# Performance work log

Measured on AMD Instinct MI355X. Metric: run time of the kernel, lower is better.

The kernel has to match this reference:

```python
import jax, jax.numpy as jnp
import numpy as np
from jax import lax

EPS = 1e-5


def _bn(x, gamma, beta, mean, var):
    # x: [B,C,H,W]; params: [C]
    inv = gamma / jnp.sqrt(var + EPS)
    return x * inv[None, :, None, None] + (beta - mean * inv)[None, :, None, None]


def _conv1x1(x, w):
    # w: [O, C] pointwise conv
    return jnp.einsum('oc,bchw->bohw', w, x)


def setup_inputs() -> dict:
    dim, num_heads = 256, 8
    B, H, W = 4, 40, 40
    key = jax.random.key(0)
    ks = jax.random.split(key, 12)
    inp = {
        'x': jax.random.normal(ks[0], (B, dim, H, W), jnp.float32),
        # qkv: Conv(dim, 2*dim, k=1) = conv1x1 (no bias) + BN + SiLU
        'qkv_w': jax.random.normal(ks[1], (2 * dim, dim), jnp.float32) * 0.05,
        'qkv_gamma': jax.random.uniform(ks[2], (2 * dim,), jnp.float32, 0.5, 1.5),
        'qkv_beta': jax.random.normal(ks[3], (2 * dim,), jnp.float32) * 0.05,
        'qkv_mean': jax.random.normal(ks[4], (2 * dim,), jnp.float32) * 0.05,
        'qkv_var': jax.random.uniform(ks[5], (2 * dim,), jnp.float32, 0.5, 1.5),
        # proj: Conv(dim, dim, k=1)
        'proj_w': jax.random.normal(ks[6], (dim, dim), jnp.float32) * 0.05,
        'proj_gamma': jax.random.uniform(ks[7], (dim,), jnp.float32, 0.5, 1.5),
        'proj_beta': jax.random.normal(ks[8], (dim,), jnp.float32) * 0.05,
        'proj_mean': jax.random.normal(ks[9], (dim,), jnp.float32) * 0.05,
        'proj_var': jax.random.uniform(ks[10], (dim,), jnp.float32, 0.5, 1.5),
        # pe: depthwise 3x3 conv (groups=dim, no bias) + BN (no activation)
        'pe_w': jax.random.normal(ks[11], (dim, 1, 3, 3), jnp.float32) * 0.1,
        'pe_gamma': jax.random.uniform(jax.random.fold_in(key, 100), (dim,), jnp.float32, 0.5, 1.5),
        'pe_beta': jax.random.normal(jax.random.fold_in(key, 101), (dim,), jnp.float32) * 0.05,
        'pe_mean': jax.random.normal(jax.random.fold_in(key, 102), (dim,), jnp.float32) * 0.05,
        'pe_var': jax.random.uniform(jax.random.fold_in(key, 103), (dim,), jnp.float32, 0.5, 1.5),
    }
    return inp


def reference(x, qkv_w, qkv_gamma, qkv_beta, qkv_mean, qkv_var,
              proj_w, proj_gamma, proj_beta, proj_mean, proj_var,
              pe_w, pe_gamma, pe_beta, pe_mean, pe_var):
    B, C, H, W = x.shape
    num_heads = 8
    head_dim = C // num_heads
    N = H * W

    # positional encoding: depthwise 3x3 conv + BN
    pe = lax.conv_general_dilated(
        x, pe_w, window_strides=(1, 1), padding='SAME',
        feature_group_count=C, dimension_numbers=('NCHW', 'OIHW', 'NCHW'))
    pe = _bn(pe, pe_gamma, pe_beta, pe_mean, pe_var)

    # qkv: 1x1 conv + BN + SiLU, then split into q, k along channels
    qkv = jax.nn.silu(_bn(_conv1x1(x, qkv_w), qkv_gamma, qkv_beta, qkv_mean, qkv_var))
    q, k = qkv[:, :C], qkv[:, C:]
    v = x + pe

    # reshape to heads: q,v -> [B,h,N,d]; k -> [B,h,d,N]
    q = q.reshape(B, num_heads, head_dim, N).transpose(0, 1, 3, 2)
    k = k.reshape(B, num_heads, head_dim, N)
    v = v.reshape(B, num_heads, head_dim, N).transpose(0, 1, 3, 2)

    scale = head_dim ** (-0.5)
    attn = jnp.einsum('bhnd,bhdm->bhnm', q, k) * scale  # [B,h,N,N]
    attn = jax.nn.softmax(attn, axis=-1)
    out = jnp.einsum('bhnm,bhmd->bhnd', attn, v)        # [B,h,N,d]
    out = out.transpose(0, 1, 3, 2).reshape(B, C, H, W)

    # proj: 1x1 conv + BN + SiLU
    return jax.nn.silu(_bn(_conv1x1(out, proj_w), proj_gamma, proj_beta, proj_mean, proj_var))
```

## Files before the change

kernel.cpp:

```cpp
#include <hip/hip_runtime.h>
#include <hip/hip_bf16.h>

typedef __attribute__((ext_vector_type(8))) short short8;
typedef __attribute__((ext_vector_type(4))) float f32x4;

__device__ __forceinline__ unsigned short f2bf(float f){
    union { float f; unsigned u; } uf; uf.f = f;
    unsigned u = uf.u;
    u += 0x7FFFu + ((u >> 16) & 1u);
    return (unsigned short)(u >> 16);
}
__device__ __forceinline__ int pack2(float a, float b){
    union { float f; unsigned u; } ua, ub; ua.f = a; ub.f = b;
    unsigned x = ua.u; x += 0x7FFFu + ((x >> 16) & 1u);
    unsigned y = ub.u; y += 0x7FFFu + ((y >> 16) & 1u);
    return (int)((x >> 16) | (y & 0xFFFF0000u));
}
__device__ __forceinline__ unsigned cvtpk(float lo, float hi){
    unsigned r;
    asm("v_cvt_pk_bf16_f32 %0, %1, %2" : "=v"(r) : "v"(lo), "v"(hi));
    return r;
}
__device__ __forceinline__ float fexp2(float x){
    return __builtin_amdgcn_exp2f(x);
}

#define N_SPATIAL 1600
#define QSCALE_LOG2E 0.25506601f
#define LSTR 40

__global__ __launch_bounds__(256) void k_head(const float* __restrict__ x,
                                              const float* __restrict__ pw,
                                              const float* __restrict__ pg,
                                              const float* __restrict__ pb,
                                              const float* __restrict__ pm,
                                              const float* __restrict__ pv,
                                              unsigned short* __restrict__ x_t,
                                              unsigned short* __restrict__ v_mf){
    __shared__ float xs[32][163];
    int bi = blockIdx.x;
    int t = threadIdx.x;
    if (bi < 200){
        int b = bi / 50, nc = bi % 50;
        int n0 = nc * 32;
        int c = t;
        unsigned short vals[32];
        const float* src = x + ((size_t)(b*256 + c))*N_SPATIAL + n0;
        #pragma unroll
        for (int j=0;j<8;j++){
            float4 f = *reinterpret_cast<const float4*>(src + j*4);
            vals[j*4+0] = f2bf(f.x); vals[j*4+1] = f2bf(f.y);
            vals[j*4+2] = f2bf(f.z); vals[j*4+3] = f2bf(f.w);
        }
        unsigned short* dst = x_t + ((size_t)b*N_SPATIAL + n0)*256 + c;
        #pragma unroll
        for (int j=0;j<32;j++) dst[(size_t)j*256] = vals[j];
        return;
    }
    int pbi = bi - 200;
    int b = pbi/200, h=(pbi/25)%8, kt=pbi%25;
    int winStart = kt*64 - 48;
    const float* xbase = x + ((size_t)(b*256 + h*32))*N_SPATIAL;
    #pragma unroll
    for (int i=0;i<20;i++){
        int idx = t + i*256;
        int row = idx / 160, col = idx - row*160;
        int n = winStart + col;
        float val = ((unsigned)n < 1600u) ? xbase[(size_t)row*N_SPATIAL + n] : 0.f;
        xs[row][col] = val;
    }
    __syncthreads();

    int f = t>>6, lane = t&63, ql = lane&15, lg = lane>>4;
    int d = (f>>1)*16 + ql;
    int c = h*32 + d;
    float inv = pg[c]*rsqrtf(pv[c]+1e-5f);
    float bias = pb[c]-pm[c]*inv;
    const float* w9 = pw + c*9;
    float w00=w9[0],w01=w9[1],w02=w9[2],w10=w9[3],w11=w9[4],w12=w9[5],w20=w9[6],w21=w9[7],w22=w9[8];
    const float* xr = xs[d];
    union { unsigned short u[8]; int4 i4; } vals;
    #pragma unroll
    for (int j=0;j<8;j++){
        int key = (f&1)*32 + (j>>2)*16 + 4*lg + (j&3);
        int n = kt*64 + key;
        int hh = n/40, ww = n - hh*40;
        int col = key + 48;
        float acc = 0.f;
        if (hh > 0){
            if (ww > 0)  acc += xr[col-41]*w00;
                         acc += xr[col-40]*w01;
            if (ww < 39) acc += xr[col-39]*w02;
        }
        if (ww > 0)  acc += xr[col-1]*w10;
                     acc += xr[col]*w11;
        if (ww < 39) acc += xr[col+1]*w12;
        if (hh < 39){
            if (ww > 0)  acc += xr[col+39]*w20;
                         acc += xr[col+40]*w21;
            if (ww < 39) acc += xr[col+41]*w22;
        }
        float out = xr[col] + acc*inv + bias;
        vals.u[j] = f2bf(out);
    }
    *reinterpret_cast<int4*>(v_mf + ((size_t)(pbi*4 + f)*64 + lane)*8) = vals.i4;
}

__global__ __launch_bounds__(256) void k_qkv2(const unsigned short* __restrict__ x_t,
                                              const float* __restrict__ wq,
                                              const float* __restrict__ g,
                                              const float* __restrict__ be,
                                              const float* __restrict__ mu,
                                              const float* __restrict__ va,
                                              unsigned short* __restrict__ qk_t){
    __shared__ alignas(16) unsigned short a_lds[64*LSTR];
    __shared__ alignas(16) unsigned short b_lds[64*LSTR];
    int bi = blockIdx.x;
    int b = bi / 200, ot = (bi/25) % 8, nt = bi % 25;
    int o0 = ot*64, n0 = nt*64;
    int tid = threadIdx.x, w = tid>>6, lane = tid&63;
    int row = tid>>2, col8 = (tid&3)*8;
    int ql = lane&15, lg = lane>>4;
    f32x4 acc[4];
    #pragma unroll
    for (int t=0;t<4;t++) acc[t] = (f32x4){0.f,0.f,0.f,0.f};
    const float* asrc = wq + (size_t)(o0+row)*256 + col8;
    const unsigned short* bsrc = x_t + ((size_t)b*N_SPATIAL + n0 + row)*256 + col8;
    for (int k0=0; k0<256; k0+=32){
        float4 f0 = *reinterpret_cast<const float4*>(asrc + k0);
        float4 f1 = *reinterpret_cast<const float4*>(asrc + k0 + 4);
        int4 av; av.x = pack2(f0.x,f0.y); av.y = pack2(f0.z,f0.w);
                 av.z = pack2(f1.x,f1.y); av.w = pack2(f1.z,f1.w);
        *reinterpret_cast<int4*>(&a_lds[row*LSTR + col8]) = av;
        *reinterpret_cast<int4*>(&b_lds[row*LSTR + col8]) = *reinterpret_cast<const int4*>(bsrc + k0);
        __syncthreads();
        short8 af = *reinterpret_cast<const short8*>(&a_lds[(16*w + ql)*LSTR + lg*8]);
        #pragma unroll
        for (int t=0;t<4;t++){
            short8 bf = *reinterpret_cast<const short8*>(&b_lds[(16*t + ql)*LSTR + lg*8]);
            acc[t] = __builtin_amdgcn_mfma_f32_16x16x32_bf16(af, bf, acc[t], 0, 0, 0);
        }
        __syncthreads();
    }
    int ob = o0 + 16*w + 4*lg;
    int grp = ob >> 5, d0 = ob & 31;
    float invr[4], b2r[4];
    #pragma unroll
    for (int r=0;r<4;r++){
        int o = ob + r;
        invr[r] = g[o] * rsqrtf(va[o] + 1e-5f);
        b2r[r]  = be[o] - mu[o]*invr[r];
    }
    float qs = (ob < 256) ? QSCALE_LOG2E : 1.0f;
    unsigned short* dstb = qk_t + ((size_t)(b*16 + grp)*N_SPATIAL)*32 + d0;
    #pragma unroll
    for (int t=0;t<4;t++){
        int n = n0 + 16*t + ql;
        float y[4];
        #pragma unroll
        for (int r=0;r<4;r++){
            float z = acc[t][r]*invr[r] + b2r[r];
            y[r] = (z / (1.f + __expf(-z))) * qs;
        }
        uint2 wv = make_uint2((unsigned)pack2(y[0],y[1]), (unsigned)pack2(y[2],y[3]));
        *reinterpret_cast<uint2*>(dstb + (size_t)n*32) = wv;
    }
}

__global__ __launch_bounds__(512) void k_attn7(const unsigned short* __restrict__ qk_t,
                                               const unsigned short* __restrict__ v_mf,
                                               unsigned short* __restrict__ ao_t){
    __shared__ alignas(16) unsigned short k_lds[3][64*40];
    __shared__ alignas(16) unsigned short v_lds[3][2048];
    int l = blockIdx.x;
    int xc = l & 7, j = l >> 3;
    int gg = xc + 8*(j/25);
    int bi = 25*gg + (j%25);
    int b = gg >> 3, h = gg & 7, qt = bi % 25;
    int tid = threadIdx.x, w = tid>>6, lane = tid&63;

    const unsigned short* ksrc = qk_t + ((size_t)(b*16+8+h)*N_SPATIAL)*32;
    const unsigned short* vms  = v_mf + (size_t)(b*200 + h*25)*2048;

    if (w < 4){
        int ql = lane&15, lg = lane>>4;
        int nq = qt*64 + w*16 + ql;
        const unsigned short* qsrc = qk_t + ((size_t)(b*16+h)*N_SPATIAL)*32;
        short8 qf = *reinterpret_cast<const short8*>(qsrc + (size_t)nq*32 + lg*8);
        f32x4 o0 = (f32x4){0.f,0.f,0.f,0.f};
        f32x4 o1 = (f32x4){0.f,0.f,0.f,0.f};
        float Sp = 0.f;

        asm volatile("" ::: "memory");
        __builtin_amdgcn_s_barrier();
        asm volatile("" ::: "memory");

        int cur = 0;
        for (int kt = 0; kt < 25; ++kt){
            const unsigned short* kb = &k_lds[cur][0];
            const unsigned short* vb = &v_lds[cur][0];
            short8 ka0 = *reinterpret_cast<const short8*>(kb + (size_t)( 0 + ql)*40 + lg*8);
            short8 ka1 = *reinterpret_cast<const short8*>(kb + (size_t)(16 + ql)*40 + lg*8);
            short8 ka2 = *reinterpret_cast<const short8*>(kb + (size_t)(32 + ql)*40 + lg*8);
            short8 ka3 = *reinterpret_cast<const short8*>(kb + (size_t)(48 + ql)*40 + lg*8);

            f32x4 z = (f32x4){0.f,0.f,0.f,0.f};
            f32x4 p0 = __builtin_amdgcn_mfma_f32_16x16x32_bf16(ka0, qf, z, 0,0,0);
            f32x4 p1 = __builtin_amdgcn_mfma_f32_16x16x32_bf16(ka1, qf, z, 0,0,0);
            f32x4 p2 = __builtin_amdgcn_mfma_f32_16x16x32_bf16(ka2, qf, z, 0,0,0);
            f32x4 p3 = __builtin_amdgcn_mfma_f32_16x16x32_bf16(ka3, qf, z, 0,0,0);

            #pragma unroll
            for (int r=0;r<4;r++){
                p0[r] = fexp2(p0[r]);
                p1[r] = fexp2(p1[r]);
                p2[r] = fexp2(p2[r]);
                p3[r] = fexp2(p3[r]);
            }
            Sp += ((p0[0]+p0[1])+(p0[2]+p0[3])) + ((p1[0]+p1[1])+(p1[2]+p1[3]))
                + ((p2[0]+p2[1])+(p2[2]+p2[3])) + ((p3[0]+p3[1])+(p3[2]+p3[3]));

            union { int4 i; short8 s8; } pb0, pb1;
            pb0.i = make_int4((int)cvtpk(p0[0],p0[1]), (int)cvtpk(p0[2],p0[3]),
                              (int)cvtpk(p1[0],p1[1]), (int)cvtpk(p1[2],p1[3]));
            pb1.i = make_int4((int)cvtpk(p2[0],p2[1]), (int)cvtpk(p2[2],p2[3]),
                              (int)cvtpk(p3[0],p3[1]), (int)cvtpk(p3[2],p3[3]));

            short8 va0 = *reinterpret_cast<const short8*>(vb +    0 + lane*8);
            short8 va1 = *reinterpret_cast<const short8*>(vb +  512 + lane*8);
            short8 va2 = *reinterpret_cast<const short8*>(vb + 1024 + lane*8);
            short8 va3 = *reinterpret_cast<const short8*>(vb + 1536 + lane*8);

            o0 = __builtin_amdgcn_mfma_f32_16x16x32_bf16(va0, pb0.s8, o0, 0,0,0);
            o0 = __builtin_amdgcn_mfma_f32_16x16x32_bf16(va1, pb1.s8, o0, 0,0,0);
            o1 = __builtin_amdgcn_mfma_f32_16x16x32_bf16(va2, pb0.s8, o1, 0,0,0);
            o1 = __builtin_amdgcn_mfma_f32_16x16x32_bf16(va3, pb1.s8, o1, 0,0,0);

            asm volatile("" ::: "memory");
            __builtin_amdgcn_s_barrier();
            asm volatile("" ::: "memory");
            cur = (cur==2) ? 0 : cur+1;
        }

        Sp += __shfl_xor(Sp, 16);
        Sp += __shfl_xor(Sp, 32);
        float inv = 1.f / Sp;
        size_t rowoff = ((size_t)b*N_SPATIAL + nq)*256 + h*32;
        uint2 w0 = make_uint2((unsigned)pack2(o0[0]*inv, o0[1]*inv),
                              (unsigned)pack2(o0[2]*inv, o0[3]*inv));
        *reinterpret_cast<uint2*>(ao_t + rowoff + 4*lg) = w0;
        uint2 w1 = make_uint2((unsigned)pack2(o1[0]*inv, o1[1]*inv),
                              (unsigned)pack2(o1[2]*inv, o1[3]*inv));
        *reinterpret_cast<uint2*>(ao_t + rowoff + 16 + 4*lg) = w1;
    } else {
        int pi = tid & 255;
        const unsigned short* kg = ksrc + pi*8;
        const unsigned short* vg = vms  + pi*8;
        unsigned short* kd = &k_lds[0][0] + (pi>>2)*40 + (pi&3)*8;
        unsigned short* vd = &v_lds[0][0] + pi*8;

        int4 a0 = *reinterpret_cast<const int4*>(kg);
        int4 b0 = *reinterpret_cast<const int4*>(vg);
        *reinterpret_cast<int4*>(kd) = a0;
        *reinterpret_cast<int4*>(vd) = b0;
        int4 a1 = *reinterpret_cast<const int4*>(kg + 2048);
        int4 b1 = *reinterpret_cast<const int4*>(vg + 2048);
        *reinterpret_cast<int4*>(kd + 2560) = a1;
        *reinterpret_cast<int4*>(vd + 2048) = b1;
        int4 hk = *reinterpret_cast<const int4*>(kg + 4096);
        int4 hv = *reinterpret_cast<const int4*>(vg + 4096);
        asm volatile("s_waitcnt lgkmcnt(0)" ::: "memory");
        __builtin_amdgcn_s_barrier();
        asm volatile("" ::: "memory");

        int wb = 2;
        for (int kt = 0; kt < 25; ++kt){
            if (kt < 23){
                *reinterpret_cast<int4*>(kd + wb*2560) = hk;
                *reinterpret_cast<int4*>(vd + wb*2048) = hv;
            }
            if (kt < 22){
                hk = *reinterpret_cast<const int4*>(kg + (size_t)(kt+3)*2048);
                hv = *reinterpret_cast<const int4*>(vg + (size_t)(kt+3)*2048);
            }
            asm volatile("s_waitcnt lgkmcnt(0)" ::: "memory");
            __builtin_amdgcn_s_barrier();
            asm volatile("" ::: "memory");
            wb = (wb==2) ? 0 : wb+1;
        }
    }
}

__global__ __launch_bounds__(256) void k_proj2(const unsigned short* __restrict__ ao_t,
                                               const float* __restrict__ wp,
                                               const float* __restrict__ g,
                                               const float* __restrict__ be,
                                               const float* __restrict__ mu,
                                               const float* __restrict__ va,
                                               float* __restrict__ out){
    __shared__ alignas(16) unsigned short a_lds[64*LSTR];
    __shared__ alignas(16) unsigned short b_lds[64*LSTR];
    int bi = blockIdx.x;
    int b = bi / 100, ot = (bi/25) % 4, nt = bi % 25;
    int o0 = ot*64, n0 = nt*64;
    int tid = threadIdx.x, w = tid>>6, lane = tid&63;
    int row = tid>>2, col8 = (tid&3)*8;
    int ql = lane&15, lg = lane>>4;
    f32x4 acc[4];
    #pragma unroll
    for (int t=0;t<4;t++) acc[t] = (f32x4){0.f,0.f,0.f,0.f};
    const float* asrc = wp + (size_t)(o0+row)*256 + col8;
    const unsigned short* bsrc = ao_t + ((size_t)b*N_SPATIAL + n0 + row)*256 + col8;
    for (int k0=0; k0<256; k0+=32){
        float4 f0 = *reinterpret_cast<const float4*>(asrc + k0);
        float4 f1 = *reinterpret_cast<const float4*>(asrc + k0 + 4);
        int4 av; av.x = pack2(f0.x,f0.y); av.y = pack2(f0.z,f0.w);
                 av.z = pack2(f1.x,f1.y); av.w = pack2(f1.z,f1.w);
        *reinterpret_cast<int4*>(&a_lds[row*LSTR + col8]) = av;
        *reinterpret_cast<int4*>(&b_lds[row*LSTR + col8]) = *reinterpret_cast<const int4*>(bsrc + k0);
        __syncthreads();
        short8 af = *reinterpret_cast<const short8*>(&a_lds[(16*w + ql)*LSTR + lg*8]);
        #pragma unroll
        for (int t=0;t<4;t++){
            short8 bf = *reinterpret_cast<const short8*>(&b_lds[(16*t + ql)*LSTR + lg*8]);
            acc[t] = __builtin_amdgcn_mfma_f32_16x16x32_bf16(af, bf, acc[t], 0, 0, 0);
        }
        __syncthreads();
    }
    #pragma unroll
    for (int r=0;r<4;r++){
        int o = o0 + 16*w + lg*4 + r;
        float inv = g[o] * rsqrtf(va[o] + 1e-5f);
        float b2  = be[o] - mu[o]*inv;
        float* dst = out + ((size_t)(b*256 + o))*N_SPATIAL;
        #pragma unroll
        for (int t=0;t<4;t++){
            int n = n0 + 16*t + ql;
            float z = acc[t][r]*inv + b2;
            float y = z / (1.f + __expf(-z));
            dst[n] = y;
        }
    }
}

extern "C" void kernel_launch(void* const* d_in, const int* in_sizes, int n_in,
                              void* d_out, int out_size, void* d_ws, size_t ws_size,
                              hipStream_t stream) {
    const float* x      = (const float*)d_in[0];
    const float* qkv_w  = (const float*)d_in[1];
    const float* qkv_g  = (const float*)d_in[2];
    const float* qkv_b  = (const float*)d_in[3];
    const float* qkv_m  = (const float*)d_in[4];
    const float* qkv_v  = (const float*)d_in[5];
    const float* proj_w = (const float*)d_in[6];
    const float* proj_g = (const float*)d_in[7];
    const float* proj_b = (const float*)d_in[8];
    const float* proj_m = (const float*)d_in[9];
    const float* proj_v = (const float*)d_in[10];
    const float* pe_w   = (const float*)d_in[11];
    const float* pe_g   = (const float*)d_in[12];
    const float* pe_b   = (const float*)d_in[13];
    const float* pe_m   = (const float*)d_in[14];
    const float* pe_v   = (const float*)d_in[15];

    char* ws = (char*)d_ws;
    unsigned short* x_t  = (unsigned short*)(ws);
    unsigned short* v_mf = (unsigned short*)(ws + 3276800);
    unsigned short* qk_t = (unsigned short*)(ws + 6553600);
    unsigned short* ao_t = (unsigned short*)(ws + 13107200);
    float* outp = (float*)d_out;

    k_head <<<1000,256, 0, stream>>>(x, pe_w, pe_g, pe_b, pe_m, pe_v, x_t, v_mf);
    k_qkv2 <<<800, 256, 0, stream>>>(x_t, qkv_w, qkv_g, qkv_b, qkv_m, qkv_v, qk_t);
    k_attn7<<<800, 512, 0, stream>>>(qk_t, v_mf, ao_t);
    k_proj2<<<400, 256, 0, stream>>>(ao_t, proj_w, proj_g, proj_b, proj_m, proj_v, outp);
}
```

Before: 59.22 us.

## Stage GEMM K in two 128-wide halves with register prefetch in qkv/proj

```diff
diff --git a/kernel.cpp b/kernel.cpp
--- a/kernel.cpp
+++ b/kernel.cpp
@@ -27,7 +27,7 @@
 
 #define N_SPATIAL 1600
 #define QSCALE_LOG2E 0.25506601f
-#define LSTR 40
+#define GSTR 136
 
 __global__ __launch_bounds__(256) void k_head(const float* __restrict__ x,
                                               const float* __restrict__ pw,
@@ -106,42 +106,93 @@
     *reinterpret_cast<int4*>(v_mf + ((size_t)(pbi*4 + f)*64 + lane)*8) = vals.i4;
 }
 
-__global__ __launch_bounds__(256) void k_qkv2(const unsigned short* __restrict__ x_t,
+__global__ __launch_bounds__(256) void k_qkv3(const unsigned short* __restrict__ x_t,
                                               const float* __restrict__ wq,
                                               const float* __restrict__ g,
                                               const float* __restrict__ be,
                                               const float* __restrict__ mu,
                                               const float* __restrict__ va,
                                               unsigned short* __restrict__ qk_t){
-    __shared__ alignas(16) unsigned short a_lds[64*LSTR];
-    __shared__ alignas(16) unsigned short b_lds[64*LSTR];
+    __shared__ alignas(16) unsigned short a_lds[64*GSTR];
+    __shared__ alignas(16) unsigned short b_lds[64*GSTR];
     int bi = blockIdx.x;
     int b = bi / 200, ot = (bi/25) % 8, nt = bi % 25;
     int o0 = ot*64, n0 = nt*64;
     int tid = threadIdx.x, w = tid>>6, lane = tid&63;
-    int row = tid>>2, col8 = (tid&3)*8;
     int ql = lane&15, lg = lane>>4;
+    int arow = (tid>>5)*2;
+    int aseg = lane&31;
+    int brow4 = (tid>>4);
+    int bseg = lane&15;
+
+    const float* wbase = wq + (size_t)o0*256;
+    const unsigned short* xbase = x_t + ((size_t)b*N_SPATIAL + n0)*256;
+
     f32x4 acc[4];
     #pragma unroll
     for (int t=0;t<4;t++) acc[t] = (f32x4){0.f,0.f,0.f,0.f};
-    const float* asrc = wq + (size_t)(o0+row)*256 + col8;
-    const unsigned short* bsrc = x_t + ((size_t)b*N_SPATIAL + n0 + row)*256 + col8;
-    for (int k0=0; k0<256; k0+=32){
-        float4 f0 = *reinterpret_cast<const float4*>(asrc + k0);
-        float4 f1 = *reinterpret_cast<const float4*>(asrc + k0 + 4);
-        int4 av; av.x = pack2(f0.x,f0.y); av.y = pack2(f0.z,f0.w);
-                 av.z = pack2(f1.x,f1.y); av.w = pack2(f1.z,f1.w);
-        *reinterpret_cast<int4*>(&a_lds[row*LSTR + col8]) = av;
-        *reinterpret_cast<int4*>(&b_lds[row*LSTR + col8]) = *reinterpret_cast<const int4*>(bsrc + k0);
-        __syncthreads();
-        short8 af = *reinterpret_cast<const short8*>(&a_lds[(16*w + ql)*LSTR + lg*8]);
+
+    #pragma unroll
+    for (int i=0;i<8;i++){
+        int row = (tid>>5) + i*8;
+        float4 fv = *reinterpret_cast<const float4*>(wbase + (size_t)row*256 + aseg*4);
+        *reinterpret_cast<uint2*>(&a_lds[row*GSTR + aseg*4]) =
+            make_uint2((unsigned)pack2(fv.x,fv.y), (unsigned)pack2(fv.z,fv.w));
+    }
+    #pragma unroll
+    for (int i=0;i<4;i++){
+        int row = brow4 + i*16;
+        *reinterpret_cast<int4*>(&b_lds[row*GSTR + bseg*8]) =
+            *reinterpret_cast<const int4*>(xbase + (size_t)row*256 + bseg*8);
+    }
+    __syncthreads();
+
+    float4 pa[8]; int4 pbv[4];
+    #pragma unroll
+    for (int i=0;i<8;i++){
+        int row = (tid>>5) + i*8;
+        pa[i] = *reinterpret_cast<const float4*>(wbase + (size_t)row*256 + 128 + aseg*4);
+    }
+    #pragma unroll
+    for (int i=0;i<4;i++){
+        int row = brow4 + i*16;
+        pbv[i] = *reinterpret_cast<const int4*>(xbase + (size_t)row*256 + 128 + bseg*8);
+    }
+
+    #pragma unroll
+    for (int k0=0; k0<128; k0+=32){
+        short8 af = *reinterpret_cast<const short8*>(&a_lds[(16*w + ql)*GSTR + k0 + lg*8]);
         #pragma unroll
         for (int t=0;t<4;t++){
-            short8 bf = *reinterpret_cast<const short8*>(&b_lds[(16*t + ql)*LSTR + lg*8]);
+            short8 bf = *reinterpret_cast<const short8*>(&b_lds[(16*t + ql)*GSTR + k0 + lg*8]);
             acc[t] = __builtin_amdgcn_mfma_f32_16x16x32_bf16(af, bf, acc[t], 0, 0, 0);
         }
-        __syncthreads();
-    }
+    }
+    __syncthreads();
+
+    #pragma unroll
+    for (int i=0;i<8;i++){
+        int row = (tid>>5) + i*8;
+        *reinterpret_cast<uint2*>(&a_lds[row*GSTR + aseg*4]) =
+            make_uint2((unsigned)pack2(pa[i].x,pa[i].y), (unsigned)pack2(pa[i].z,pa[i].w));
+    }
+    #pragma unroll
+    for (int i=0;i<4;i++){
+        int row = brow4 + i*16;
+        *reinterpret_cast<int4*>(&b_lds[row*GSTR + bseg*8]) = pbv[i];
+    }
+    __syncthreads();
+
+    #pragma unroll
+    for (int k0=0; k0<128; k0+=32){
+        short8 af = *reinterpret_cast<const short8*>(&a_lds[(16*w + ql)*GSTR + k0 + lg*8]);
+        #pragma unroll
+        for (int t=0;t<4;t++){
+            short8 bf = *reinterpret_cast<const short8*>(&b_lds[(16*t + ql)*GSTR + k0 + lg*8]);
+            acc[t] = __builtin_amdgcn_mfma_f32_16x16x32_bf16(af, bf, acc[t], 0, 0, 0);
+        }
+    }
+
     int ob = o0 + 16*w + 4*lg;
     int grp = ob >> 5, d0 = ob & 31;
     float invr[4], b2r[4];
@@ -291,42 +342,92 @@
     }
 }
 
-__global__ __launch_bounds__(256) void k_proj2(const unsigned short* __restrict__ ao_t,
+__global__ __launch_bounds__(256) void k_proj3(const unsigned short* __restrict__ ao_t,
                                                const float* __restrict__ wp,
                                                const float* __restrict__ g,
                                                const float* __restrict__ be,
                                                const float* __restrict__ mu,
                                                const float* __restrict__ va,
                                                float* __restrict__ out){
-    __shared__ alignas(16) unsigned short a_lds[64*LSTR];
-    __shared__ alignas(16) unsigned short b_lds[64*LSTR];
+    __shared__ alignas(16) unsigned short a_lds[64*GSTR];
+    __shared__ alignas(16) unsigned short b_lds[64*GSTR];
     int bi = blockIdx.x;
     int b = bi / 100, ot = (bi/25) % 4, nt = bi % 25;
     int o0 = ot*64, n0 = nt*64;
     int tid = threadIdx.x, w = tid>>6, lane = tid&63;
-    int row = tid>>2, col8 = (tid&3)*8;
     int ql = lane&15, lg = lane>>4;
+    int aseg = lane&31;
+    int brow4 = (tid>>4);
+    int bseg = lane&15;
+
+    const float* wbase = wp + (size_t)o0*256;
+    const unsigned short* xbase = ao_t + ((size_t)b*N_SPATIAL + n0)*256;
+
     f32x4 acc[4];
     #pragma unroll
     for (int t=0;t<4;t++) acc[t] = (f32x4){0.f,0.f,0.f,0.f};
-    const float* asrc = wp + (size_t)(o0+row)*256 + col8;
-    const unsigned short* bsrc = ao_t + ((size_t)b*N_SPATIAL + n0 + row)*256 + col8;
-    for (int k0=0; k0<256; k0+=32){
-        float4 f0 = *reinterpret_cast<const float4*>(asrc + k0);
-        float4 f1 = *reinterpret_cast<const float4*>(asrc + k0 + 4);
-        int4 av; av.x = pack2(f0.x,f0.y); av.y = pack2(f0.z,f0.w);
-                 av.z = pack2(f1.x,f1.y); av.w = pack2(f1.z,f1.w);
-        *reinterpret_cast<int4*>(&a_lds[row*LSTR + col8]) = av;
-        *reinterpret_cast<int4*>(&b_lds[row*LSTR + col8]) = *reinterpret_cast<const int4*>(bsrc + k0);
-        __syncthreads();
-        short8 af = *reinterpret_cast<const short8*>(&a_lds[(16*w + ql)*LSTR + lg*8]);
+
+    #pragma unroll
+    for (int i=0;i<8;i++){
+        int row = (tid>>5) + i*8;
+        float4 fv = *reinterpret_cast<const float4*>(wbase + (size_t)row*256 + aseg*4);
+        *reinterpret_cast<uint2*>(&a_lds[row*GSTR + aseg*4]) =
+            make_uint2((unsigned)pack2(fv.x,fv.y), (unsigned)pack2(fv.z,fv.w));
+    }
+    #pragma unroll
+    for (int i=0;i<4;i++){
+        int row = brow4 + i*16;
+        *reinterpret_cast<int4*>(&b_lds[row*GSTR + bseg*8]) =
+            *reinterpret_cast<const int4*>(xbase + (size_t)row*256 + bseg*8);
+    }
+    __syncthreads();
+
+    float4 pa[8]; int4 pbv[4];
+    #pragma unroll
+    for (int i=0;i<8;i++){
+        int row = (tid>>5) + i*8;
+        pa[i] = *reinterpret_cast<const float4*>(wbase + (size_t)row*256 + 128 + aseg*4);
+    }
+    #pragma unroll
+    for (int i=0;i<4;i++){
+        int row = brow4 + i*16;
+        pbv[i] = *reinterpret_cast<const int4*>(xbase + (size_t)row*256 + 128 + bseg*8);
+    }
+
+    #pragma unroll
+    for (int k0=0; k0<128; k0+=32){
+        short8 af = *reinterpret_cast<const short8*>(&a_lds[(16*w + ql)*GSTR + k0 + lg*8]);
         #pragma unroll
         for (int t=0;t<4;t++){
-            short8 bf = *reinterpret_cast<const short8*>(&b_lds[(16*t + ql)*LSTR + lg*8]);
+            short8 bf = *reinterpret_cast<const short8*>(&b_lds[(16*t + ql)*GSTR + k0 + lg*8]);
             acc[t] = __builtin_amdgcn_mfma_f32_16x16x32_bf16(af, bf, acc[t], 0, 0, 0);
         }
-        __syncthreads();
-    }
+    }
+    __syncthreads();
+
+    #pragma unroll
+    for (int i=0;i<8;i++){
+        int row = (tid>>5) + i*8;
+        *reinterpret_cast<uint2*>(&a_lds[row*GSTR + aseg*4]) =
+            make_uint2((unsigned)pack2(pa[i].x,pa[i].y), (unsigned)pack2(pa[i].z,pa[i].w));
+    }
+    #pragma unroll
+    for (int i=0;i<4;i++){
+        int row = brow4 + i*16;
+        *reinterpret_cast<int4*>(&b_lds[row*GSTR + bseg*8]) = pbv[i];
+    }
+    __syncthreads();
+
+    #pragma unroll
+    for (int k0=0; k0<128; k0+=32){
+        short8 af = *reinterpret_cast<const short8*>(&a_lds[(16*w + ql)*GSTR + k0 + lg*8]);
+        #pragma unroll
+        for (int t=0;t<4;t++){
+            short8 bf = *reinterpret_cast<const short8*>(&b_lds[(16*t + ql)*GSTR + k0 + lg*8]);
+            acc[t] = __builtin_amdgcn_mfma_f32_16x16x32_bf16(af, bf, acc[t], 0, 0, 0);
+        }
+    }
+
     #pragma unroll
     for (int r=0;r<4;r++){
         int o = o0 + 16*w + lg*4 + r;
@@ -371,7 +472,7 @@
     float* outp = (float*)d_out;
 
     k_head <<<1000,256, 0, stream>>>(x, pe_w, pe_g, pe_b, pe_m, pe_v, x_t, v_mf);
-    k_qkv2 <<<800, 256, 0, stream>>>(x_t, qkv_w, qkv_g, qkv_b, qkv_m, qkv_v, qk_t);
+    k_qkv3 <<<800, 256, 0, stream>>>(x_t, qkv_w, qkv_g, qkv_b, qkv_m, qkv_v, qk_t);
     k_attn7<<<800, 512, 0, stream>>>(qk_t, v_mf, ao_t);
-    k_proj2<<<400, 256, 0, stream>>>(ao_t, proj_w, proj_g, proj_b, proj_m, proj_v, outp);
-}
+    k_proj3<<<400, 256, 0, stream>>>(ao_t, proj_w, proj_g, proj_b, proj_m, proj_v, outp);
+}
```

Measured after the change: 62.85 us. 1.06x slower.

## Store K in MFMA fragment layout and stream K/V via direct global-to-LDS loads

Applied to the files above, without the earlier changes.

```diff
diff --git a/kernel.cpp b/kernel.cpp
--- a/kernel.cpp
+++ b/kernel.cpp
@@ -23,6 +23,12 @@
 }
 __device__ __forceinline__ float fexp2(float x){
     return __builtin_amdgcn_exp2f(x);
+}
+__device__ __forceinline__ void load_lds16(const void* g, void* l){
+    __builtin_amdgcn_global_load_lds(
+        (const __attribute__((address_space(1))) unsigned int*)g,
+        (__attribute__((address_space(3))) unsigned int*)l,
+        16, 0, 0);
 }
 
 #define N_SPATIAL 1600
@@ -112,7 +118,8 @@
                                               const float* __restrict__ be,
                                               const float* __restrict__ mu,
                                               const float* __restrict__ va,
-                                              unsigned short* __restrict__ qk_t){
+                                              unsigned short* __restrict__ q_t,
+                                              unsigned short* __restrict__ k_mf){
     __shared__ alignas(16) unsigned short a_lds[64*LSTR];
     __shared__ alignas(16) unsigned short b_lds[64*LSTR];
     int bi = blockIdx.x;
@@ -143,7 +150,7 @@
         __syncthreads();
     }
     int ob = o0 + 16*w + 4*lg;
-    int grp = ob >> 5, d0 = ob & 31;
+    int d0 = ob & 31;
     float invr[4], b2r[4];
     #pragma unroll
     for (int r=0;r<4;r++){
@@ -151,144 +158,135 @@
         invr[r] = g[o] * rsqrtf(va[o] + 1e-5f);
         b2r[r]  = be[o] - mu[o]*invr[r];
     }
-    float qs = (ob < 256) ? QSCALE_LOG2E : 1.0f;
-    unsigned short* dstb = qk_t + ((size_t)(b*16 + grp)*N_SPATIAL)*32 + d0;
-    #pragma unroll
-    for (int t=0;t<4;t++){
-        int n = n0 + 16*t + ql;
-        float y[4];
-        #pragma unroll
-        for (int r=0;r<4;r++){
-            float z = acc[t][r]*invr[r] + b2r[r];
-            y[r] = (z / (1.f + __expf(-z))) * qs;
-        }
-        uint2 wv = make_uint2((unsigned)pack2(y[0],y[1]), (unsigned)pack2(y[2],y[3]));
-        *reinterpret_cast<uint2*>(dstb + (size_t)n*32) = wv;
-    }
-}
-
-__global__ __launch_bounds__(512) void k_attn7(const unsigned short* __restrict__ qk_t,
+    if (ob < 256){
+        int grp = ob >> 5;
+        unsigned short* dstb = q_t + ((size_t)(b*8 + grp)*N_SPATIAL)*32 + d0;
+        #pragma unroll
+        for (int t=0;t<4;t++){
+            int n = n0 + 16*t + ql;
+            float y[4];
+            #pragma unroll
+            for (int r=0;r<4;r++){
+                float z = acc[t][r]*invr[r] + b2r[r];
+                y[r] = (z / (1.f + __expf(-z))) * QSCALE_LOG2E;
+            }
+            *reinterpret_cast<uint2*>(dstb + (size_t)n*32) =
+                make_uint2((unsigned)pack2(y[0],y[1]), (unsigned)pack2(y[2],y[3]));
+        }
+    } else {
+        int hh = (ob>>5) - 8;
+        size_t kbase = (size_t)((b*8+hh)*25)*2048;
+        #pragma unroll
+        for (int t=0;t<4;t++){
+            int n = n0 + 16*t + ql;
+            int kt = n>>6, tf = (n>>4)&3, qr = n&15;
+            float y[4];
+            #pragma unroll
+            for (int r=0;r<4;r++){
+                float z = acc[t][r]*invr[r] + b2r[r];
+                y[r] = z / (1.f + __expf(-z));
+            }
+            size_t off = kbase + (size_t)kt*2048 + tf*512 + ((d0>>3)*16 + qr)*8 + (d0&7);
+            *reinterpret_cast<uint2*>(k_mf + off) =
+                make_uint2((unsigned)pack2(y[0],y[1]), (unsigned)pack2(y[2],y[3]));
+        }
+    }
+}
+
+__global__ __launch_bounds__(256) void k_attn8(const unsigned short* __restrict__ q_t,
+                                               const unsigned short* __restrict__ k_mf,
                                                const unsigned short* __restrict__ v_mf,
                                                unsigned short* __restrict__ ao_t){
-    __shared__ alignas(16) unsigned short k_lds[3][64*40];
-    __shared__ alignas(16) unsigned short v_lds[3][2048];
+    __shared__ alignas(16) unsigned short k_lds[4][2048];
+    __shared__ alignas(16) unsigned short v_lds[4][2048];
     int l = blockIdx.x;
     int xc = l & 7, j = l >> 3;
     int gg = xc + 8*(j/25);
-    int bi = 25*gg + (j%25);
-    int b = gg >> 3, h = gg & 7, qt = bi % 25;
+    int b = gg >> 3, h = gg & 7, qt = j % 25;
     int tid = threadIdx.x, w = tid>>6, lane = tid&63;
-
-    const unsigned short* ksrc = qk_t + ((size_t)(b*16+8+h)*N_SPATIAL)*32;
+    int ql = lane&15, lg = lane>>4;
+    int nq = qt*64 + w*16 + ql;
+
+    const unsigned short* qsrc = q_t + ((size_t)(b*8+h)*N_SPATIAL)*32;
+    const unsigned short* kms  = k_mf + (size_t)((b*8+h)*25)*2048;
     const unsigned short* vms  = v_mf + (size_t)(b*200 + h*25)*2048;
 
-    if (w < 4){
-        int ql = lane&15, lg = lane>>4;
-        int nq = qt*64 + w*16 + ql;
-        const unsigned short* qsrc = qk_t + ((size_t)(b*16+h)*N_SPATIAL)*32;
-        short8 qf = *reinterpret_cast<const short8*>(qsrc + (size_t)nq*32 + lg*8);
-        f32x4 o0 = (f32x4){0.f,0.f,0.f,0.f};
-        f32x4 o1 = (f32x4){0.f,0.f,0.f,0.f};
-        float Sp = 0.f;
-
-        asm volatile("" ::: "memory");
+    short8 qf = *reinterpret_cast<const short8*>(qsrc + (size_t)nq*32 + lg*8);
+
+    const unsigned short* kg = kms + w*512 + lane*8;
+    const unsigned short* vg = vms + w*512 + lane*8;
+
+    load_lds16(kg,        &k_lds[0][w*512]);
+    load_lds16(vg,        &v_lds[0][w*512]);
+    load_lds16(kg + 2048, &k_lds[1][w*512]);
+    load_lds16(vg + 2048, &v_lds[1][w*512]);
+
+    f32x4 o0 = (f32x4){0.f,0.f,0.f,0.f};
+    f32x4 o1 = (f32x4){0.f,0.f,0.f,0.f};
+    float Sp = 0.f;
+
+    for (int kt = 0; kt < 25; ++kt){
+        if (kt+2 < 25){
+            int bidx = (kt+2)&3;
+            load_lds16(kg + (size_t)(kt+2)*2048, &k_lds[bidx][w*512]);
+            load_lds16(vg + (size_t)(kt+2)*2048, &v_lds[bidx][w*512]);
+        }
+        if (kt < 23)       asm volatile("s_waitcnt vmcnt(4)" ::: "memory");
+        else if (kt == 23) asm volatile("s_waitcnt vmcnt(2)" ::: "memory");
+        else               asm volatile("s_waitcnt vmcnt(0)" ::: "memory");
         __builtin_amdgcn_s_barrier();
         asm volatile("" ::: "memory");
 
-        int cur = 0;
-        for (int kt = 0; kt < 25; ++kt){
-            const unsigned short* kb = &k_lds[cur][0];
-            const unsigned short* vb = &v_lds[cur][0];
-            short8 ka0 = *reinterpret_cast<const short8*>(kb + (size_t)( 0 + ql)*40 + lg*8);
-            short8 ka1 = *reinterpret_cast<const short8*>(kb + (size_t)(16 + ql)*40 + lg*8);
-            short8 ka2 = *reinterpret_cast<const short8*>(kb + (size_t)(32 + ql)*40 + lg*8);
-            short8 ka3 = *reinterpret_cast<const short8*>(kb + (size_t)(48 + ql)*40 + lg*8);
-
-            f32x4 z = (f32x4){0.f,0.f,0.f,0.f};
-            f32x4 p0 = __builtin_amdgcn_mfma_f32_16x16x32_bf16(ka0, qf, z, 0,0,0);
-            f32x4 p1 = __builtin_amdgcn_mfma_f32_16x16x32_bf16(ka1, qf, z, 0,0,0);
-            f32x4 p2 = __builtin_amdgcn_mfma_f32_16x16x32_bf16(ka2, qf, z, 0,0,0);
-            f32x4 p3 = __builtin_amdgcn_mfma_f32_16x16x32_bf16(ka3, qf, z, 0,0,0);
-
-            #pragma unroll
-            for (int r=0;r<4;r++){
-                p0[r] = fexp2(p0[r]);
-                p1[r] = fexp2(p1[r]);
-                p2[r] = fexp2(p2[r]);
-                p3[r] = fexp2(p3[r]);
-            }
-            Sp += ((p0[0]+p0[1])+(p0[2]+p0[3])) + ((p1[0]+p1[1])+(p1[2]+p1[3]))
-                + ((p2[0]+p2[1])+(p2[2]+p2[3])) + ((p3[0]+p3[1])+(p3[2]+p3[3]));
-
-            union { int4 i; short8 s8; } pb0, pb1;
-            pb0.i = make_int4((int)cvtpk(p0[0],p0[1]), (int)cvtpk(p0[2],p0[3]),
-                              (int)cvtpk(p1[0],p1[1]), (int)cvtpk(p1[2],p1[3]));
-            pb1.i = make_int4((int)cvtpk(p2[0],p2[1]), (int)cvtpk(p2[2],p2[3]),
-                              (int)cvtpk(p3[0],p3[1]), (int)cvtpk(p3[2],p3[3]));
-
-            short8 va0 = *reinterpret_cast<const short8*>(vb +    0 + lane*8);
-            short8 va1 = *reinterpret_cast<const short8*>(vb +  512 + lane*8);
-            short8 va2 = *reinterpret_cast<const short8*>(vb + 1024 + lane*8);
-            short8 va3 = *reinterpret_cast<const short8*>(vb + 1536 + lane*8);
-
-            o0 = __builtin_amdgcn_mfma_f32_16x16x32_bf16(va0, pb0.s8, o0, 0,0,0);
-            o0 = __builtin_amdgcn_mfma_f32_16x16x32_bf16(va1, pb1.s8, o0, 0,0,0);
-            o1 = __builtin_amdgcn_mfma_f32_16x16x32_bf16(va2, pb0.s8, o1, 0,0,0);
-            o1 = __builtin_amdgcn_mfma_f32_16x16x32_bf16(va3, pb1.s8, o1, 0,0,0);
-
-            asm volatile("" ::: "memory");
-            __builtin_amdgcn_s_barrier();
-            asm volatile("" ::: "memory");
-            cur = (cur==2) ? 0 : cur+1;
-        }
-
-        Sp += __shfl_xor(Sp, 16);
-        Sp += __shfl_xor(Sp, 32);
-        float inv = 1.f / Sp;
-        size_t rowoff = ((size_t)b*N_SPATIAL + nq)*256 + h*32;
-        uint2 w0 = make_uint2((unsigned)pack2(o0[0]*inv, o0[1]*inv),
-                              (unsigned)pack2(o0[2]*inv, o0[3]*inv));
-        *reinterpret_cast<uint2*>(ao_t + rowoff + 4*lg) = w0;
-        uint2 w1 = make_uint2((unsigned)pack2(o1[0]*inv, o1[1]*inv),
-                              (unsigned)pack2(o1[2]*inv, o1[3]*inv));
-        *reinterpret_cast<uint2*>(ao_t + rowoff + 16 + 4*lg) = w1;
-    } else {
-        int pi = tid & 255;
-        const unsigned short* kg = ksrc + pi*8;
-        const unsigned short* vg = vms  + pi*8;
-        unsigned short* kd = &k_lds[0][0] + (pi>>2)*40 + (pi&3)*8;
-        unsigned short* vd = &v_lds[0][0] + pi*8;
-
-        int4 a0 = *reinterpret_cast<const int4*>(kg);
-        int4 b0 = *reinterpret_cast<const int4*>(vg);
-        *reinterpret_cast<int4*>(kd) = a0;
-        *reinterpret_cast<int4*>(vd) = b0;
-        int4 a1 = *reinterpret_cast<const int4*>(kg + 2048);
-        int4 b1 = *reinterpret_cast<const int4*>(vg + 2048);
-        *reinterpret_cast<int4*>(kd + 2560) = a1;
-        *reinterpret_cast<int4*>(vd + 2048) = b1;
-        int4 hk = *reinterpret_cast<const int4*>(kg + 4096);
-        int4 hv = *reinterpret_cast<const int4*>(vg + 4096);
-        asm volatile("s_waitcnt lgkmcnt(0)" ::: "memory");
-        __builtin_amdgcn_s_barrier();
-        asm volatile("" ::: "memory");
-
-        int wb = 2;
-        for (int kt = 0; kt < 25; ++kt){
-            if (kt < 23){
-                *reinterpret_cast<int4*>(kd + wb*2560) = hk;
-                *reinterpret_cast<int4*>(vd + wb*2048) = hv;
-            }
-            if (kt < 22){
-                hk = *reinterpret_cast<const int4*>(kg + (size_t)(kt+3)*2048);
-                hv = *reinterpret_cast<const int4*>(vg + (size_t)(kt+3)*2048);
-            }
-            asm volatile("s_waitcnt lgkmcnt(0)" ::: "memory");
-            __builtin_amdgcn_s_barrier();
-            asm volatile("" ::: "memory");
-            wb = (wb==2) ? 0 : wb+1;
-        }
-    }
+        const unsigned short* kb = &k_lds[kt&3][0];
+        const unsigned short* vb = &v_lds[kt&3][0];
+        short8 ka0 = *reinterpret_cast<const short8*>(kb +    0 + lane*8);
+        short8 ka1 = *reinterpret_cast<const short8*>(kb +  512 + lane*8);
+        short8 ka2 = *reinterpret_cast<const short8*>(kb + 1024 + lane*8);
+        short8 ka3 = *reinterpret_cast<const short8*>(kb + 1536 + lane*8);
+
+        f32x4 z = (f32x4){0.f,0.f,0.f,0.f};
+        f32x4 p0 = __builtin_amdgcn_mfma_f32_16x16x32_bf16(ka0, qf, z, 0,0,0);
+        f32x4 p1 = __builtin_amdgcn_mfma_f32_16x16x32_bf16(ka1, qf, z, 0,0,0);
+        f32x4 p2 = __builtin_amdgcn_mfma_f32_16x16x32_bf16(ka2, qf, z, 0,0,0);
+        f32x4 p3 = __builtin_amdgcn_mfma_f32_16x16x32_bf16(ka3, qf, z, 0,0,0);
+
+        #pragma unroll
+        for (int r=0;r<4;r++){
+            p0[r] = fexp2(p0[r]);
+            p1[r] = fexp2(p1[r]);
+            p2[r] = fexp2(p2[r]);
+            p3[r] = fexp2(p3[r]);
+        }
+        Sp += ((p0[0]+p0[1])+(p0[2]+p0[3])) + ((p1[0]+p1[1])+(p1[2]+p1[3]))
+            + ((p2[0]+p2[1])+(p2[2]+p2[3])) + ((p3[0]+p3[1])+(p3[2]+p3[3]));
+
+        union { int4 i; short8 s8; } pb0, pb1;
+        pb0.i = make_int4((int)cvtpk(p0[0],p0[1]), (int)cvtpk(p0[2],p0[3]),
+                          (int)cvtpk(p1[0],p1[1]), (int)cvtpk(p1[2],p1[3]));
+        pb1.i = make_int4((int)cvtpk(p2[0],p2[1]), (int)cvtpk(p2[2],p2[3]),
+                          (int)cvtpk(p3[0],p3[1]), (int)cvtpk(p3[2],p3[3]));
+
+        short8 va0 = *reinterpret_cast<const short8*>(vb +    0 + lane*8);
+        short8 va1 = *reinterpret_cast<const short8*>(vb +  512 + lane*8);
+        short8 va2 = *reinterpret_cast<const short8*>(vb + 1024 + lane*8);
+        short8 va3 = *reinterpret_cast<const short8*>(vb + 1536 + lane*8);
+
+        o0 = __builtin_amdgcn_mfma_f32_16x16x32_bf16(va0, pb0.s8, o0, 0,0,0);
+        o0 = __builtin_amdgcn_mfma_f32_16x16x32_bf16(va1, pb1.s8, o0, 0,0,0);
+        o1 = __builtin_amdgcn_mfma_f32_16x16x32_bf16(va2, pb0.s8, o1, 0,0,0);
+        o1 = __builtin_amdgcn_mfma_f32_16x16x32_bf16(va3, pb1.s8, o1, 0,0,0);
+    }
+
+    Sp += __shfl_xor(Sp, 16);
+    Sp += __shfl_xor(Sp, 32);
+    float inv = 1.f / Sp;
+    size_t rowoff = ((size_t)b*N_SPATIAL + nq)*256 + h*32;
+    uint2 w0 = make_uint2((unsigned)pack2(o0[0]*inv, o0[1]*inv),
+                          (unsigned)pack2(o0[2]*inv, o0[3]*inv));
+    *reinterpret_cast<uint2*>(ao_t + rowoff + 4*lg) = w0;
+    uint2 w1 = make_uint2((unsigned)pack2(o1[0]*inv, o1[1]*inv),
+                          (unsigned)pack2(o1[2]*inv, o1[3]*inv));
+    *reinterpret_cast<uint2*>(ao_t + rowoff + 16 + 4*lg) = w1;
 }
 
 __global__ __launch_bounds__(256) void k_proj2(const unsigned short* __restrict__ ao_t,
@@ -366,12 +364,13 @@
     char* ws = (char*)d_ws;
     unsigned short* x_t  = (unsigned short*)(ws);
     unsigned short* v_mf = (unsigned short*)(ws + 3276800);
-    unsigned short* qk_t = (unsigned short*)(ws + 6553600);
+    unsigned short* q_t  = (unsigned short*)(ws + 6553600);
+    unsigned short* k_mf = (unsigned short*)(ws + 9830400);
     unsigned short* ao_t = (unsigned short*)(ws + 13107200);
     float* outp = (float*)d_out;
 
     k_head <<<1000,256, 0, stream>>>(x, pe_w, pe_g, pe_b, pe_m, pe_v, x_t, v_mf);
-    k_qkv2 <<<800, 256, 0, stream>>>(x_t, qkv_w, qkv_g, qkv_b, qkv_m, qkv_v, qk_t);
-    k_attn7<<<800, 512, 0, stream>>>(qk_t, v_mf, ao_t);
+    k_qkv2 <<<800, 256, 0, stream>>>(x_t, qkv_w, qkv_g, qkv_b, qkv_m, qkv_v, q_t, k_mf);
+    k_attn8<<<800, 256, 0, stream>>>(q_t, k_mf, v_mf, ao_t);
     k_proj2<<<400, 256, 0, stream>>>(ao_t, proj_w, proj_g, proj_b, proj_m, proj_v, outp);
 }
```

Measured after the change: 62.21 us. +5.0%, slower.
